# Performance work log

Measured on AMD Instinct MI355X. Metric: run time of the kernel, lower is better.

## Reference

```python
import jax, jax.numpy as jnp
import numpy as np

H = 16  # n_heads

def setup_inputs() -> dict:
    key = jax.random.key(0)
    ks = jax.random.split(key, 11)
    B, L, D = 2, 2048, 1024
    w = 1.0 / np.sqrt(D).astype(np.float32)
    return {
        "query": jax.random.normal(ks[0], (B, L, D), jnp.float32),
        "key":   jax.random.normal(ks[1], (B, L, D), jnp.float32),
        "value": jax.random.normal(ks[2], (B, L, D), jnp.float32),
        "Wq": jax.random.normal(ks[3], (D, D), jnp.float32) * w,
        "bq": jax.random.normal(ks[4], (D,), jnp.float32) * 0.01,
        "Wk": jax.random.normal(ks[5], (D, D), jnp.float32) * w,
        "bk": jax.random.normal(ks[6], (D,), jnp.float32) * 0.01,
        "Wv": jax.random.normal(ks[7], (D, D), jnp.float32) * w,
        "bv": jax.random.normal(ks[8], (D,), jnp.float32) * 0.01,
        "Wo": jax.random.normal(ks[9], (D, D), jnp.float32) * w,
        "bo": jax.random.normal(ks[10], (D,), jnp.float32) * 0.01,
        "masksize": 256,
    }

def reference(query, key, value, Wq, bq, Wk, bk, Wv, bv, Wo, bo, masksize):
    B, L, D = query.shape
    d_k = D // H
    scale = 1.0 / np.sqrt(d_k).astype(np.float32)

    def proj(x, W, b):
        # nn.Linear: x @ W.T + b, then [B,L,H,d_k] -> [B,H,L,d_k]
        return (x @ W.T + b).reshape(B, L, H, d_k).transpose(0, 2, 1, 3)

    q = proj(query, Wq, bq)
    k = proj(key, Wk, bk)
    v = proj(value, Wv, bv)

    # Sliding-window float mask (faithful to original: a 0/1 FLOAT tensor is
    # passed as attn_mask to SDPA, so it is ADDED to scores, not -inf-masked).
    half = masksize // 2
    i = jnp.arange(L)[:, None]
    j = jnp.arange(L)[None, :]
    band = (jnp.abs(i - j) <= half).astype(q.dtype)  # [L, L]

    scores = jnp.einsum('bhqd,bhkd->bhqk', q, k) * scale + band  # [B,H,L,L]
    attn = jax.nn.softmax(scores, axis=-1)
    out = jnp.einsum('bhqk,bhkd->bhqd', attn, v)  # [B,H,L,d_k]
    out = out.transpose(0, 2, 1, 3).reshape(B, L, D)
    return out @ Wo.T + bo
```

## Files before the change

kernel.cpp:

```cpp
#include <hip/hip_runtime.h>
#include <hip/hip_bf16.h>

#define Hh 16
#define Ll 2048
#define Dd 1024
#define DK 64
#define Mm 4096
#define Kk 1024
#define Nn 1024

typedef short bf16x8 __attribute__((ext_vector_type(8)));
typedef float f32x4 __attribute__((ext_vector_type(4)));

static __device__ __forceinline__ unsigned short f2bf(float f) {
    union { __hip_bfloat16 b; unsigned short u; } cv;
    cv.b = __float2bfloat16(f);
    return cv.u;
}

static __device__ __forceinline__ unsigned packtr(float a, float b) {
    return __builtin_amdgcn_perm(__builtin_bit_cast(unsigned, b),
                                 __builtin_bit_cast(unsigned, a), 0x07060302u);
}

static __device__ __forceinline__ float fexp2(float x) {
    return __builtin_amdgcn_exp2f(x);
}

static __device__ __forceinline__ void glds16(const ushort* g, ushort* l) {
    __builtin_amdgcn_global_load_lds((const __attribute__((address_space(1))) unsigned int*)g,
                                     (__attribute__((address_space(3))) unsigned int*)l,
                                     16, 0, 0);
}

__global__ __launch_bounds__(256) void cast_all(
    const float* __restrict__ q, const float* __restrict__ k, const float* __restrict__ v,
    const float* __restrict__ wq, const float* __restrict__ wk, const float* __restrict__ wv,
    const float* __restrict__ wo,
    ushort* __restrict__ qb, ushort* __restrict__ kb, ushort* __restrict__ vb,
    ushort* __restrict__ wqb, ushort* __restrict__ wkb, ushort* __restrict__ wvb,
    ushort* __restrict__ wob) {
    const int bx = blockIdx.x;
    const float4* s; ushort4* d; int base;
    if      (bx <  4096) { s = (const float4*)q;  d = (ushort4*)qb;  base = 0; }
    else if (bx <  8192) { s = (const float4*)k;  d = (ushort4*)kb;  base = 4096; }
    else if (bx < 12288) { s = (const float4*)v;  d = (ushort4*)vb;  base = 8192; }
    else if (bx < 13312) { s = (const float4*)wq; d = (ushort4*)wqb; base = 12288; }
    else if (bx < 14336) { s = (const float4*)wk; d = (ushort4*)wkb; base = 13312; }
    else if (bx < 15360) { s = (const float4*)wv; d = (ushort4*)wvb; base = 14336; }
    else                 { s = (const float4*)wo; d = (ushort4*)wob; base = 15360; }
    const int i = (bx - base) * 256 + threadIdx.x;
    float4 vv = s[i];
    ushort4 o;
    o.x = f2bf(vv.x); o.y = f2bf(vv.y); o.z = f2bf(vv.z); o.w = f2bf(vv.w);
    d[i] = o;
}

__global__ __launch_bounds__(256) void gemm_qkv(
    const ushort* __restrict__ A0, const ushort* __restrict__ A1, const ushort* __restrict__ A2,
    const ushort* __restrict__ W0, const ushort* __restrict__ W1, const ushort* __restrict__ W2,
    const float* __restrict__ b0, const float* __restrict__ b1, const float* __restrict__ b2,
    ushort* __restrict__ O0, ushort* __restrict__ O1, ushort* __restrict__ OVt) {
    __shared__ __align__(16) ushort SM[2 * 128 * 32];
    ushort* As = SM;
    ushort* Bs = SM + 4096;
    const int z = blockIdx.z;
    const ushort* A = (z == 0) ? A0 : (z == 1) ? A1 : A2;
    const ushort* W = (z == 0) ? W0 : (z == 1) ? W1 : W2;
    const float* bias = (z == 0) ? b0 : (z == 1) ? b1 : b2;

    const int t = threadIdx.x;
    const int wave = t >> 6, lane = t & 63;
    const int quad = lane >> 4, l15 = lane & 15;
    const int brow = blockIdx.y * 128, bcol = blockIdx.x * 128;
    const int wr = (wave >> 1) * 64, wc = (wave & 1) * 64;
    const int gr = wave * 16 + (lane >> 2);
    const int gc = (lane & 3) * 8;

    f32x4 acc[4][4] = {};

    for (int k0 = 0; k0 < Kk; k0 += 32) {
        __syncthreads();
        glds16(A + (size_t)(brow + gr) * Kk + k0 + gc,      As + wave * 512);
        glds16(A + (size_t)(brow + 64 + gr) * Kk + k0 + gc, As + 2048 + wave * 512);
        glds16(W + (size_t)(bcol + gr) * Kk + k0 + gc,      Bs + wave * 512);
        glds16(W + (size_t)(bcol + 64 + gr) * Kk + k0 + gc, Bs + 2048 + wave * 512);
        __syncthreads();

        bf16x8 af[4], bfr[4];
#pragma unroll
        for (int i = 0; i < 4; i++)
            af[i] = *(const bf16x8*)(As + (wr + i * 16 + l15) * 32 + quad * 8);
#pragma unroll
        for (int j = 0; j < 4; j++)
            bfr[j] = *(const bf16x8*)(Bs + (wc + j * 16 + l15) * 32 + quad * 8);
#pragma unroll
        for (int i = 0; i < 4; i++)
#pragma unroll
            for (int j = 0; j < 4; j++)
                acc[i][j] = __builtin_amdgcn_mfma_f32_16x16x32_bf16(af[i], bfr[j], acc[i][j], 0, 0, 0);
    }

    if (z < 2) {
        ushort* Out = (z == 0) ? O0 : O1;
        const float oscl = (z == 0) ? 0.18033688f : 1.0f;
#pragma unroll
        for (int i = 0; i < 4; i++)
#pragma unroll
            for (int j = 0; j < 4; j++) {
                const int n = bcol + wc + j * 16 + l15;
                const float bv = bias[n];
                const int h = n >> 6, dk = n & 63;
#pragma unroll
                for (int r = 0; r < 4; r++) {
                    const int m = brow + wr + i * 16 + quad * 4 + r;
                    const int b = m >> 11, l = m & 2047;
                    Out[((size_t)(b * Hh + h) * Ll + l) * DK + dk] = f2bf((acc[i][j][r] + bv) * oscl);
                }
            }
    } else {
        ushort* T = SM;
        const int b = brow >> 11;
        const int lbase = brow & 2047;
        const int npr = (wave & 1) * 16 + l15;
#pragma unroll
        for (int j = 0; j < 4; j++) {
            __syncthreads();
            const float bv = bias[bcol + wc + j * 16 + l15];
#pragma unroll
            for (int i = 0; i < 4; i++)
#pragma unroll
                for (int r = 0; r < 4; r++) {
                    const int m = wr + i * 16 + quad * 4 + r;
                    T[npr * 136 + m] = f2bf(acc[i][j][r] + bv);
                }
            __syncthreads();
#pragma unroll
            for (int cc = 0; cc < 2; cc++) {
                const int idx = t + cc * 256;
                const int ni = idx >> 4;
                const int ms = idx & 15;
                const int n = bcol + (ni >> 4) * 64 + j * 16 + (ni & 15);
                const int hh = n >> 6, dk = n & 63;
                uint4 val = *(const uint4*)(T + ni * 136 + ms * 8);
                *(uint4*)(OVt + ((size_t)(b * Hh + hh) * DK + dk) * Ll + lbase + ms * 8) = val;
            }
        }
    }
}

__global__ __launch_bounds__(256) void attn_kernel(const ushort* __restrict__ Q,
                                                   const ushort* __restrict__ Kp,
                                                   const ushort* __restrict__ Vt,
                                                   ushort* __restrict__ Oout,
                                                   const int* __restrict__ masksize) {
    __shared__ __align__(16) ushort Ks[2 * 128 * 32];
    __shared__ __align__(16) ushort Vs[64 * 128];
    const int t = threadIdx.x;
    const int wave = t >> 6, lane = t & 63;
    const int quad = lane >> 4, l15 = lane & 15;
    const int bx = blockIdx.x;
    const int bh = bx & 31, qc = bx >> 5;
    const int q0w = qc * 128 + wave * 32;
    const int half = masksize[0] >> 1;
    const unsigned wid = (unsigned)(2 * half);

    const ushort* Qb = Q + (size_t)bh * (Ll * DK);
    const ushort* Kb = Kp + (size_t)bh * (Ll * DK);
    const ushort* Vb = Vt + (size_t)bh * (DK * Ll);

    const bf16x8 qA0 = *(const bf16x8*)(Qb + (size_t)(q0w + l15) * DK + quad * 8);
    const bf16x8 qA1 = *(const bf16x8*)(Qb + (size_t)(q0w + l15) * DK + 32 + quad * 8);
    const bf16x8 qB0 = *(const bf16x8*)(Qb + (size_t)(q0w + 16 + l15) * DK + quad * 8);
    const bf16x8 qB1 = *(const bf16x8*)(Qb + (size_t)(q0w + 16 + l15) * DK + 32 + quad * 8);

    const float C2IN  = (1.0f - 24.0f) * 1.44269504088896f;
    const float C2OUT = -24.0f * 1.44269504088896f;
    const float E1 = 2.718281828f;

    bf16x8 onesf;
#pragma unroll
    for (int j = 0; j < 8; j++) onesf[j] = (short)0x3F80;

    f32x4 OA[4] = {}, OB[4] = {};
    f32x4 SA = {}, SB = {};

    const int krow = lane >> 2;
    const int kcol8 = (lane & 3) * 8;
    const int vdl = lane >> 4;
    const int vg0 = 2 * (lane & 15);

    for (int kt = 0; kt < Ll; kt += 128) {
        __syncthreads();
        if (wave < 2) {
            const int cbase = wave * 4;
#pragma unroll
            for (int c = 0; c < 4; c++)
#pragma unroll
                for (int pan = 0; pan < 2; pan++)
                    glds16(Kb + (size_t)(kt + (cbase + c) * 16 + krow) * DK + pan * 32 + kcol8,
                           Ks + (pan * 128 + (cbase + c) * 16) * 32);
        } else {
            const int sb = (wave - 2) * 8;
#pragma unroll
            for (int i = 0; i < 8; i++) {
                const int sidx = sb + i;
                const int d = sidx * 4 + vdl;
                const int g0 = vg0 ^ (d & 30);
                glds16(Vb + (size_t)d * Ll + kt + g0 * 4, Vs + sidx * 512);
            }
        }
        __syncthreads();

        const int qlo = q0w, qhi = q0w + 31;
        const bool allout = (kt + 127 < qlo - half) || (kt > qhi + half);
        const bool allin  = (kt >= qhi - half) && (kt + 127 <= qlo + half);
        const bool uniform = allin || allout;
        const float cinit = allin ? C2IN : C2OUT;
        f32x4 cvec = {cinit, cinit, cinit, cinit};

#pragma unroll
        for (int s = 0; s < 4; s++) {
            const bf16x8 kf00 = *(const bf16x8*)(Ks + ((2 * s) * 16 + l15) * 32 + quad * 8);
            const bf16x8 kf01 = *(const bf16x8*)(Ks + 4096 + ((2 * s) * 16 + l15) * 32 + quad * 8);
            const bf16x8 kf10 = *(const bf16x8*)(Ks + ((2 * s + 1) * 16 + l15) * 32 + quad * 8);
            const bf16x8 kf11 = *(const bf16x8*)(Ks + 4096 + ((2 * s + 1) * 16 + l15) * 32 + quad * 8);
            f32x4 zA0 = __builtin_amdgcn_mfma_f32_16x16x32_bf16(kf00, qA0, cvec, 0, 0, 0);
            zA0 = __builtin_amdgcn_mfma_f32_16x16x32_bf16(kf01, qA1, zA0, 0, 0, 0);
            f32x4 zA1 = __builtin_amdgcn_mfma_f32_16x16x32_bf16(kf10, qA0, cvec, 0, 0, 0);
            zA1 = __builtin_amdgcn_mfma_f32_16x16x32_bf16(kf11, qA1, zA1, 0, 0, 0);
            f32x4 zB0 = __builtin_amdgcn_mfma_f32_16x16x32_bf16(kf00, qB0, cvec, 0, 0, 0);
            zB0 = __builtin_amdgcn_mfma_f32_16x16x32_bf16(kf01, qB1, zB0, 0, 0, 0);
            f32x4 zB1 = __builtin_amdgcn_mfma_f32_16x16x32_bf16(kf10, qB0, cvec, 0, 0, 0);
            zB1 = __builtin_amdgcn_mfma_f32_16x16x32_bf16(kf11, qB1, zB1, 0, 0, 0);

            float pA[8], pB[8];
            if (uniform) {
#pragma unroll
                for (int g = 0; g < 2; g++)
#pragma unroll
                    for (int r = 0; r < 4; r++) {
                        pA[g * 4 + r] = fexp2(g ? zA1[r] : zA0[r]);
                        pB[g * 4 + r] = fexp2(g ? zB1[r] : zB0[r]);
                    }
            } else {
                const int kb = kt + s * 32 + quad * 4 + half;
#pragma unroll
                for (int g = 0; g < 2; g++)
#pragma unroll
                    for (int r = 0; r < 4; r++) {
                        const unsigned ttA = (unsigned)(kb + g * 16 + r - (q0w + l15));
                        const unsigned ttB = (unsigned)(kb + g * 16 + r - (q0w + 16 + l15));
                        pA[g * 4 + r] = fexp2(g ? zA1[r] : zA0[r]) * (ttA <= wid ? E1 : 1.0f);
                        pB[g * 4 + r] = fexp2(g ? zB1[r] : zB0[r]) * (ttB <= wid ? E1 : 1.0f);
                    }
            }

            bf16x8 pfA, pfB;
            ((unsigned*)&pfA)[0] = packtr(pA[0], pA[1]);
            ((unsigned*)&pfA)[1] = packtr(pA[2], pA[3]);
            ((unsigned*)&pfA)[2] = packtr(pA[4], pA[5]);
            ((unsigned*)&pfA)[3] = packtr(pA[6], pA[7]);
            ((unsigned*)&pfB)[0] = packtr(pB[0], pB[1]);
            ((unsigned*)&pfB)[1] = packtr(pB[2], pB[3]);
            ((unsigned*)&pfB)[2] = packtr(pB[4], pB[5]);
            ((unsigned*)&pfB)[3] = packtr(pB[6], pB[7]);

            SA = __builtin_amdgcn_mfma_f32_16x16x32_bf16(pfA, onesf, SA, 0, 0, 0);
            SB = __builtin_amdgcn_mfma_f32_16x16x32_bf16(pfB, onesf, SB, 0, 0, 0);

#pragma unroll
            for (int i = 0; i < 4; i++) {
                const int d = i * 16 + l15;
                const int x4 = (d & 30) * 4;
                const int bi = d * 128;
                const ushort4 v1 = *(const ushort4*)(Vs + bi + (((s * 8 + quad) * 4) ^ x4));
                const ushort4 v2 = *(const ushort4*)(Vs + bi + (((s * 8 + 4 + quad) * 4) ^ x4));
                bf16x8 vc;
                *(ushort4*)&vc = v1;
                *((ushort4*)&vc + 1) = v2;
                OA[i] = __builtin_amdgcn_mfma_f32_16x16x32_bf16(pfA, vc, OA[i], 0, 0, 0);
                OB[i] = __builtin_amdgcn_mfma_f32_16x16x32_bf16(pfB, vc, OB[i], 0, 0, 0);
            }
        }
    }

    float liA[4], liB[4];
#pragma unroll
    for (int r = 0; r < 4; r++) {
        liA[r] = 1.0f / SA[r];
        liB[r] = 1.0f / SB[r];
    }

    const int b = bh >> 4, h = bh & 15;
#pragma unroll
    for (int i = 0; i < 4; i++)
#pragma unroll
        for (int r = 0; r < 4; r++) {
            const int qa = q0w + quad * 4 + r;
            Oout[((size_t)b * Ll + qa) * Dd + h * DK + i * 16 + l15] = f2bf(OA[i][r] * liA[r]);
            Oout[((size_t)b * Ll + qa + 16) * Dd + h * DK + i * 16 + l15] = f2bf(OB[i][r] * liB[r]);
        }
}

__global__ __launch_bounds__(256) void gemm_o(const ushort* __restrict__ A,
                                              const ushort* __restrict__ W,
                                              const float* __restrict__ bias,
                                              float* __restrict__ Out) {
    __shared__ __align__(16) ushort As[64 * 32];
    __shared__ __align__(16) ushort Bs[128 * 32];
    const int t = threadIdx.x;
    const int wave = t >> 6, lane = t & 63;
    const int quad = lane >> 4, l15 = lane & 15;
    const int brow = blockIdx.y * 64, bcol = blockIdx.x * 128;
    const int wr = (wave >> 1) * 32, wc = (wave & 1) * 64;
    const int gr = wave * 16 + (lane >> 2);
    const int gc = (lane & 3) * 8;

    f32x4 acc[2][4] = {};

    for (int k0 = 0; k0 < Kk; k0 += 32) {
        __syncthreads();
        glds16(A + (size_t)(brow + gr) * Kk + k0 + gc,      As + wave * 512);
        glds16(W + (size_t)(bcol + gr) * Kk + k0 + gc,      Bs + wave * 512);
        glds16(W + (size_t)(bcol + 64 + gr) * Kk + k0 + gc, Bs + 2048 + wave * 512);
        __syncthreads();

        bf16x8 af[2], bfr[4];
#pragma unroll
        for (int i = 0; i < 2; i++)
            af[i] = *(const bf16x8*)(As + (wr + i * 16 + l15) * 32 + quad * 8);
#pragma unroll
        for (int j = 0; j < 4; j++)
            bfr[j] = *(const bf16x8*)(Bs + (wc + j * 16 + l15) * 32 + quad * 8);
#pragma unroll
        for (int i = 0; i < 2; i++)
#pragma unroll
            for (int j = 0; j < 4; j++)
                acc[i][j] = __builtin_amdgcn_mfma_f32_16x16x32_bf16(af[i], bfr[j], acc[i][j], 0, 0, 0);
    }

#pragma unroll
    for (int i = 0; i < 2; i++)
#pragma unroll
        for (int j = 0; j < 4; j++) {
            const int n = bcol + wc + j * 16 + l15;
            const float bv = bias[n];
#pragma unroll
            for (int r = 0; r < 4; r++) {
                const int m = brow + wr + i * 16 + quad * 4 + r;
                Out[(size_t)m * Nn + n] = acc[i][j][r] + bv;
            }
        }
}

extern "C" void kernel_launch(void* const* d_in, const int* in_sizes, int n_in,
                              void* d_out, int out_size, void* d_ws, size_t ws_size,
                              hipStream_t stream) {
    const float* query = (const float*)d_in[0];
    const float* key   = (const float*)d_in[1];
    const float* value = (const float*)d_in[2];
    const float* Wq = (const float*)d_in[3];
    const float* bq = (const float*)d_in[4];
    const float* Wk = (const float*)d_in[5];
    const float* bk = (const float*)d_in[6];
    const float* Wv = (const float*)d_in[7];
    const float* bv = (const float*)d_in[8];
    const float* Wo = (const float*)d_in[9];
    const float* bo = (const float*)d_in[10];
    const int* masksize = (const int*)d_in[11];

    char* ws = (char*)d_ws;
    const size_t MB = 1024 * 1024;
    ushort* qb  = (ushort*)(ws + 0 * MB);
    ushort* kbf = (ushort*)(ws + 8 * MB);
    ushort* vbf = (ushort*)(ws + 16 * MB);
    ushort* wqb = (ushort*)(ws + 24 * MB);
    ushort* wkb = (ushort*)(ws + 26 * MB);
    ushort* wvb = (ushort*)(ws + 28 * MB);
    ushort* wob = (ushort*)(ws + 30 * MB);
    ushort* Qp  = (ushort*)(ws + 32 * MB);
    ushort* Kp  = (ushort*)(ws + 40 * MB);
    ushort* Vt  = (ushort*)(ws + 48 * MB);
    ushort* AO  = (ushort*)(ws + 56 * MB);

    cast_all<<<16384, 256, 0, stream>>>(query, key, value, Wq, Wk, Wv, Wo,
                                        qb, kbf, vbf, wqb, wkb, wvb, wob);

    gemm_qkv<<<dim3(8, 32, 3), 256, 0, stream>>>(qb, kbf, vbf,
                                                 wqb, wkb, wvb,
                                                 bq, bk, bv,
                                                 Qp, Kp, Vt);

    attn_kernel<<<512, 256, 0, stream>>>(Qp, Kp, Vt, AO, masksize);

    gemm_o<<<dim3(8, 64), 256, 0, stream>>>(AO, wob, bo, (float*)d_out);
}
```

Measured before the change: 224.5 us.

## Double K-step per barrier in QKV/O GEMMs and stage Q/K epilogue through LDS

Both the QKV projection and output GEMMs now load a 64-wide K slice (two 32-wide panels) per barrier pair instead of 32. This halves the number of __syncthreads per GEMM and issues more async loads per sync, at the cost of twice the shared memory. The Q/K epilogue also writes each wave's 16x64 tile into LDS and then stores it with 16-byte vector writes, replacing scattered 2-byte global stores into the head-major layout.

```diff
diff --git a/kernel.cpp b/kernel.cpp
--- a/kernel.cpp
+++ b/kernel.cpp
@@ -61,9 +61,9 @@
     const ushort* __restrict__ W0, const ushort* __restrict__ W1, const ushort* __restrict__ W2,
     const float* __restrict__ b0, const float* __restrict__ b1, const float* __restrict__ b2,
     ushort* __restrict__ O0, ushort* __restrict__ O1, ushort* __restrict__ OVt) {
-    __shared__ __align__(16) ushort SM[2 * 128 * 32];
+    __shared__ __align__(16) ushort SM[4 * 128 * 32];
     ushort* As = SM;
-    ushort* Bs = SM + 4096;
+    ushort* Bs = SM + 8192;
     const int z = blockIdx.z;
     const ushort* A = (z == 0) ? A0 : (z == 1) ? A1 : A2;
     const ushort* W = (z == 0) ? W0 : (z == 1) ? W1 : W2;
@@ -74,50 +74,68 @@
     const int quad = lane >> 4, l15 = lane & 15;
     const int brow = blockIdx.y * 128, bcol = blockIdx.x * 128;
     const int wr = (wave >> 1) * 64, wc = (wave & 1) * 64;
-    const int gr = wave * 16 + (lane >> 2);
-    const int gc = (lane & 3) * 8;
+    const int c2r = lane >> 2;
+    const int c2c = (lane & 3) * 8;
 
     f32x4 acc[4][4] = {};
 
-    for (int k0 = 0; k0 < Kk; k0 += 32) {
-        __syncthreads();
-        glds16(A + (size_t)(brow + gr) * Kk + k0 + gc,      As + wave * 512);
-        glds16(A + (size_t)(brow + 64 + gr) * Kk + k0 + gc, As + 2048 + wave * 512);
-        glds16(W + (size_t)(bcol + gr) * Kk + k0 + gc,      Bs + wave * 512);
-        glds16(W + (size_t)(bcol + 64 + gr) * Kk + k0 + gc, Bs + 2048 + wave * 512);
-        __syncthreads();
-
-        bf16x8 af[4], bfr[4];
-#pragma unroll
-        for (int i = 0; i < 4; i++)
-            af[i] = *(const bf16x8*)(As + (wr + i * 16 + l15) * 32 + quad * 8);
-#pragma unroll
-        for (int j = 0; j < 4; j++)
-            bfr[j] = *(const bf16x8*)(Bs + (wc + j * 16 + l15) * 32 + quad * 8);
-#pragma unroll
-        for (int i = 0; i < 4; i++)
+    for (int k0 = 0; k0 < Kk; k0 += 64) {
+        __syncthreads();
+#pragma unroll
+        for (int halfc = 0; halfc < 2; halfc++) {
+            const int c = wave * 2 + halfc;
+#pragma unroll
+            for (int p = 0; p < 2; p++) {
+                glds16(A + (size_t)(brow + c * 16 + c2r) * Kk + k0 + p * 32 + c2c,
+                       As + p * 4096 + (c * 16) * 32);
+                glds16(W + (size_t)(bcol + c * 16 + c2r) * Kk + k0 + p * 32 + c2c,
+                       Bs + p * 4096 + (c * 16) * 32);
+            }
+        }
+        __syncthreads();
+
+#pragma unroll
+        for (int p = 0; p < 2; p++) {
+            bf16x8 af[4], bfr[4];
+#pragma unroll
+            for (int i = 0; i < 4; i++)
+                af[i] = *(const bf16x8*)(As + p * 4096 + (wr + i * 16 + l15) * 32 + quad * 8);
 #pragma unroll
             for (int j = 0; j < 4; j++)
-                acc[i][j] = __builtin_amdgcn_mfma_f32_16x16x32_bf16(af[i], bfr[j], acc[i][j], 0, 0, 0);
+                bfr[j] = *(const bf16x8*)(Bs + p * 4096 + (wc + j * 16 + l15) * 32 + quad * 8);
+#pragma unroll
+            for (int i = 0; i < 4; i++)
+#pragma unroll
+                for (int j = 0; j < 4; j++)
+                    acc[i][j] = __builtin_amdgcn_mfma_f32_16x16x32_bf16(af[i], bfr[j], acc[i][j], 0, 0, 0);
+        }
     }
 
     if (z < 2) {
         ushort* Out = (z == 0) ? O0 : O1;
         const float oscl = (z == 0) ? 0.18033688f : 1.0f;
-#pragma unroll
-        for (int i = 0; i < 4; i++)
+        const int b = brow >> 11;
+        const int lbase = (brow & 2047) + wr;
+        const int h = (bcol + wc) >> 6;
+        ushort* T = SM + wave * 1280;
+        __syncthreads();
+#pragma unroll
+        for (int i = 0; i < 4; i++) {
 #pragma unroll
             for (int j = 0; j < 4; j++) {
-                const int n = bcol + wc + j * 16 + l15;
-                const float bv = bias[n];
-                const int h = n >> 6, dk = n & 63;
-#pragma unroll
-                for (int r = 0; r < 4; r++) {
-                    const int m = brow + wr + i * 16 + quad * 4 + r;
-                    const int b = m >> 11, l = m & 2047;
-                    Out[((size_t)(b * Hh + h) * Ll + l) * DK + dk] = f2bf((acc[i][j][r] + bv) * oscl);
-                }
-            }
+                const float bv = bias[bcol + wc + j * 16 + l15];
+#pragma unroll
+                for (int r = 0; r < 4; r++)
+                    T[(quad * 4 + r) * 80 + j * 16 + l15] = f2bf((acc[i][j][r] + bv) * oscl);
+            }
+            const int r8 = lane >> 3, c8 = lane & 7;
+#pragma unroll
+            for (int pass = 0; pass < 2; pass++) {
+                const uint4 val = *(const uint4*)(T + (pass * 8 + r8) * 80 + c8 * 8);
+                const int l = lbase + i * 16 + pass * 8 + r8;
+                *(uint4*)(Out + ((size_t)(b * Hh + h) * Ll + l) * DK + c8 * 8) = val;
+            }
+        }
     } else {
         ushort* T = SM;
         const int b = brow >> 11;
@@ -307,37 +325,48 @@
                                               const ushort* __restrict__ W,
                                               const float* __restrict__ bias,
                                               float* __restrict__ Out) {
-    __shared__ __align__(16) ushort As[64 * 32];
-    __shared__ __align__(16) ushort Bs[128 * 32];
+    __shared__ __align__(16) ushort As[2 * 64 * 32];
+    __shared__ __align__(16) ushort Bs[2 * 128 * 32];
     const int t = threadIdx.x;
     const int wave = t >> 6, lane = t & 63;
     const int quad = lane >> 4, l15 = lane & 15;
     const int brow = blockIdx.y * 64, bcol = blockIdx.x * 128;
     const int wr = (wave >> 1) * 32, wc = (wave & 1) * 64;
-    const int gr = wave * 16 + (lane >> 2);
-    const int gc = (lane & 3) * 8;
+    const int c2r = lane >> 2;
+    const int c2c = (lane & 3) * 8;
 
     f32x4 acc[2][4] = {};
 
-    for (int k0 = 0; k0 < Kk; k0 += 32) {
-        __syncthreads();
-        glds16(A + (size_t)(brow + gr) * Kk + k0 + gc,      As + wave * 512);
-        glds16(W + (size_t)(bcol + gr) * Kk + k0 + gc,      Bs + wave * 512);
-        glds16(W + (size_t)(bcol + 64 + gr) * Kk + k0 + gc, Bs + 2048 + wave * 512);
-        __syncthreads();
-
-        bf16x8 af[2], bfr[4];
-#pragma unroll
-        for (int i = 0; i < 2; i++)
-            af[i] = *(const bf16x8*)(As + (wr + i * 16 + l15) * 32 + quad * 8);
-#pragma unroll
-        for (int j = 0; j < 4; j++)
-            bfr[j] = *(const bf16x8*)(Bs + (wc + j * 16 + l15) * 32 + quad * 8);
-#pragma unroll
-        for (int i = 0; i < 2; i++)
+    for (int k0 = 0; k0 < Kk; k0 += 64) {
+        __syncthreads();
+#pragma unroll
+        for (int p = 0; p < 2; p++) {
+            glds16(A + (size_t)(brow + wave * 16 + c2r) * Kk + k0 + p * 32 + c2c,
+                   As + p * 2048 + (wave * 16) * 32);
+#pragma unroll
+            for (int halfc = 0; halfc < 2; halfc++) {
+                const int c = wave * 2 + halfc;
+                glds16(W + (size_t)(bcol + c * 16 + c2r) * Kk + k0 + p * 32 + c2c,
+                       Bs + p * 4096 + (c * 16) * 32);
+            }
+        }
+        __syncthreads();
+
+#pragma unroll
+        for (int p = 0; p < 2; p++) {
+            bf16x8 af[2], bfr[4];
+#pragma unroll
+            for (int i = 0; i < 2; i++)
+                af[i] = *(const bf16x8*)(As + p * 2048 + (wr + i * 16 + l15) * 32 + quad * 8);
 #pragma unroll
             for (int j = 0; j < 4; j++)
-                acc[i][j] = __builtin_amdgcn_mfma_f32_16x16x32_bf16(af[i], bfr[j], acc[i][j], 0, 0, 0);
+                bfr[j] = *(const bf16x8*)(Bs + p * 4096 + (wc + j * 16 + l15) * 32 + quad * 8);
+#pragma unroll
+            for (int i = 0; i < 2; i++)
+#pragma unroll
+                for (int j = 0; j < 4; j++)
+                    acc[i][j] = __builtin_amdgcn_mfma_f32_16x16x32_bf16(af[i], bfr[j], acc[i][j], 0, 0, 0);
+        }
     }
 
 #pragma unroll
```

Measured after the change: 229.6 us. 2.3% more time.

## Stage QKV epilogue through LDS and split-K output GEMM with atomics

Applied to the files above, without the earlier changes.

The Q/K projection epilogue now writes bf16 results into a per-wave LDS tile and then stores them as 16-byte vectors along each head row, replacing scattered 2-byte global writes. The output projection GEMM moves to 128x128 tiles with a 2-way split-K over blockIdx.z. Partial sums are combined with float atomicAdd into an output zeroed by a memset, and only the first split adds the bias. This trades more reuse per tile and better store coalescing for atomic traffic, an extra memset, and nondeterministic summation order.

```diff
diff --git a/kernel.cpp b/kernel.cpp
--- a/kernel.cpp
+++ b/kernel.cpp
@@ -104,20 +104,28 @@
     if (z < 2) {
         ushort* Out = (z == 0) ? O0 : O1;
         const float oscl = (z == 0) ? 0.18033688f : 1.0f;
-#pragma unroll
-        for (int i = 0; i < 4; i++)
+        const int b = brow >> 11;
+        const int lbase = (brow & 2047) + wr;
+        const int h = (bcol + wc) >> 6;
+        ushort* T = SM + wave * 1280;
+        __syncthreads();
+#pragma unroll
+        for (int i = 0; i < 4; i++) {
 #pragma unroll
             for (int j = 0; j < 4; j++) {
-                const int n = bcol + wc + j * 16 + l15;
-                const float bv = bias[n];
-                const int h = n >> 6, dk = n & 63;
-#pragma unroll
-                for (int r = 0; r < 4; r++) {
-                    const int m = brow + wr + i * 16 + quad * 4 + r;
-                    const int b = m >> 11, l = m & 2047;
-                    Out[((size_t)(b * Hh + h) * Ll + l) * DK + dk] = f2bf((acc[i][j][r] + bv) * oscl);
-                }
-            }
+                const float bv = bias[bcol + wc + j * 16 + l15];
+#pragma unroll
+                for (int r = 0; r < 4; r++)
+                    T[(quad * 4 + r) * 80 + j * 16 + l15] = f2bf((acc[i][j][r] + bv) * oscl);
+            }
+            const int r8 = lane >> 3, c8 = lane & 7;
+#pragma unroll
+            for (int pass = 0; pass < 2; pass++) {
+                const uint4 val = *(const uint4*)(T + (pass * 8 + r8) * 80 + c8 * 8);
+                const int l = lbase + i * 16 + pass * 8 + r8;
+                *(uint4*)(Out + ((size_t)(b * Hh + h) * Ll + l) * DK + c8 * 8) = val;
+            }
+        }
     } else {
         ushort* T = SM;
         const int b = brow >> 11;
@@ -307,49 +315,52 @@
                                               const ushort* __restrict__ W,
                                               const float* __restrict__ bias,
                                               float* __restrict__ Out) {
-    __shared__ __align__(16) ushort As[64 * 32];
+    __shared__ __align__(16) ushort As[128 * 32];
     __shared__ __align__(16) ushort Bs[128 * 32];
     const int t = threadIdx.x;
     const int wave = t >> 6, lane = t & 63;
     const int quad = lane >> 4, l15 = lane & 15;
-    const int brow = blockIdx.y * 64, bcol = blockIdx.x * 128;
-    const int wr = (wave >> 1) * 32, wc = (wave & 1) * 64;
+    const int brow = blockIdx.y * 128, bcol = blockIdx.x * 128;
+    const int ks = blockIdx.z * 512;
+    const int wr = (wave >> 1) * 64, wc = (wave & 1) * 64;
     const int gr = wave * 16 + (lane >> 2);
     const int gc = (lane & 3) * 8;
 
-    f32x4 acc[2][4] = {};
-
-    for (int k0 = 0; k0 < Kk; k0 += 32) {
+    f32x4 acc[4][4] = {};
+
+    for (int k0 = ks; k0 < ks + 512; k0 += 32) {
         __syncthreads();
         glds16(A + (size_t)(brow + gr) * Kk + k0 + gc,      As + wave * 512);
+        glds16(A + (size_t)(brow + 64 + gr) * Kk + k0 + gc, As + 2048 + wave * 512);
         glds16(W + (size_t)(bcol + gr) * Kk + k0 + gc,      Bs + wave * 512);
         glds16(W + (size_t)(bcol + 64 + gr) * Kk + k0 + gc, Bs + 2048 + wave * 512);
         __syncthreads();
 
-        bf16x8 af[2], bfr[4];
-#pragma unroll
-        for (int i = 0; i < 2; i++)
+        bf16x8 af[4], bfr[4];
+#pragma unroll
+        for (int i = 0; i < 4; i++)
             af[i] = *(const bf16x8*)(As + (wr + i * 16 + l15) * 32 + quad * 8);
 #pragma unroll
         for (int j = 0; j < 4; j++)
             bfr[j] = *(const bf16x8*)(Bs + (wc + j * 16 + l15) * 32 + quad * 8);
 #pragma unroll
-        for (int i = 0; i < 2; i++)
+        for (int i = 0; i < 4; i++)
 #pragma unroll
             for (int j = 0; j < 4; j++)
                 acc[i][j] = __builtin_amdgcn_mfma_f32_16x16x32_bf16(af[i], bfr[j], acc[i][j], 0, 0, 0);
     }
 
-#pragma unroll
-    for (int i = 0; i < 2; i++)
+    const bool addb = (blockIdx.z == 0);
+#pragma unroll
+    for (int i = 0; i < 4; i++)
 #pragma unroll
         for (int j = 0; j < 4; j++) {
             const int n = bcol + wc + j * 16 + l15;
-            const float bv = bias[n];
+            const float bv = addb ? bias[n] : 0.0f;
 #pragma unroll
             for (int r = 0; r < 4; r++) {
                 const int m = brow + wr + i * 16 + quad * 4 + r;
-                Out[(size_t)m * Nn + n] = acc[i][j][r] + bv;
+                atomicAdd(&Out[(size_t)m * Nn + n], acc[i][j][r] + bv);
             }
         }
 }
@@ -384,6 +395,8 @@
     ushort* Vt  = (ushort*)(ws + 48 * MB);
     ushort* AO  = (ushort*)(ws + 56 * MB);
 
+    hipMemsetAsync(d_out, 0, (size_t)Mm * Nn * sizeof(float), stream);
+
     cast_all<<<16384, 256, 0, stream>>>(query, key, value, Wq, Wk, Wv, Wo,
                                         qb, kbf, vbf, wqb, wkb, wvb, wob);
 
@@ -394,5 +407,5 @@
 
     attn_kernel<<<512, 256, 0, stream>>>(Qp, Kp, Vt, AO, masksize);
 
-    gemm_o<<<dim3(8, 64), 256, 0, stream>>>(AO, wob, bo, (float*)d_out);
-}
+    gemm_o<<<dim3(8, 32, 2), 256, 0, stream>>>(AO, wob, bo, (float*)d_out);
+}
```

Measured after the change: 260.0 us. +15.8%, slower.
